# Performance work log

Hardware: AMD Instinct MI355X
Metric: run time of the kernel (lower is better)

## Reference

```python
import jax, jax.numpy as jnp
import numpy as np

N_NODES = 50000
N_EDGES = 800000
IN_F = 512
OUT_F = 96
ALPHA = 0.1
ITERATIONS = 10
AVG_DEG = 16


def setup_inputs() -> dict:
    key = jax.random.key(0)
    k1, k2, k3, k4, k5 = jax.random.split(key, 5)
    x = jax.random.normal(k1, (N_NODES, IN_F), dtype=jnp.float32)
    # xavier_uniform with gain=1.414 over [IN_F, OUT_F]
    limit = 1.414 * np.sqrt(6.0 / (IN_F + OUT_F))
    weight = jax.random.uniform(k2, (IN_F, OUT_F), dtype=jnp.float32,
                                minval=-limit, maxval=limit)
    edge_src = jax.random.randint(k3, (N_EDGES,), 0, N_NODES, dtype=jnp.int32)
    edge_dst = jax.random.randint(k4, (N_EDGES,), 0, N_NODES, dtype=jnp.int32)
    # values scaled like a row-normalized adjacency for stable propagation
    edge_val = jax.random.uniform(k5, (N_EDGES,), dtype=jnp.float32) / AVG_DEG
    return {"x": x, "weight": weight, "edge_src": edge_src,
            "edge_dst": edge_dst, "edge_val": edge_val}


def _spmm(edge_src, edge_dst, edge_val, h):
    # out[i] = sum_{edges e with dst=i} val[e] * h[src[e]]
    gathered = h[edge_src] * edge_val[:, None]          # [E, OUT_F]
    return jax.ops.segment_sum(gathered, edge_dst, num_segments=N_NODES)


def reference(x, weight, edge_src, edge_dst, edge_val):
    support = x @ weight                                 # [N, OUT_F]
    prev = support
    def body(_, s):
        s = _spmm(edge_src, edge_dst, edge_val, s) * (1.0 - ALPHA) + prev * ALPHA
        return jax.nn.relu(s)
    return jax.lax.fori_loop(0, ITERATIONS, body, support)
```

## Files before the change

### kernel.cpp

```cpp
#include <hip/hip_runtime.h>

typedef unsigned int   uint;
typedef unsigned short ushort;
typedef __attribute__((ext_vector_type(8))) short bf16x8;
typedef __attribute__((ext_vector_type(4))) float f32x4;

#define N_NODES 50000
#define N_EDGES 800000
#define IN_F    512
#define OUT_F   96
#define SCAN_BLOCKS 196
#define TPN 12

__device__ __forceinline__ float bflo(uint u) { return __uint_as_float(u << 16); }
__device__ __forceinline__ float bfhi(uint u) { return __uint_as_float(u & 0xffff0000u); }
__device__ __forceinline__ uint f2bf(float x) {
    uint u = __float_as_uint(x);
    return (u + 0x7fffu + ((u >> 16) & 1u)) >> 16;
}
__device__ __forceinline__ uint pack2bf(float lo, float hi) {
    return f2bf(lo) | (f2bf(hi) << 16);
}

__global__ __launch_bounds__(256) void wt_kernel(const float* __restrict__ w,
                                                 ushort* __restrict__ wTp) {
    int t = blockIdx.x * 256 + threadIdx.x;
    if (t < IN_F * OUT_F) {
        int k = t / OUT_F, c = t - k * OUT_F;
        wTp[(size_t)(k >> 5) * (OUT_F * 32) + c * 32 + (k & 31)] =
            (ushort)f2bf(w[t]);
    }
}

__global__ __launch_bounds__(64) void gemm_kernel(const float* __restrict__ x,
                                                  const ushort* __restrict__ wTp,
                                                  ushort* __restrict__ supB) {
    const int lane = threadIdx.x;
    const int m    = lane & 15;
    const int quad = lane >> 4;

    const int row  = blockIdx.x * 16 + m;
    const int arow = (row < N_NODES) ? row : (N_NODES - 1);
    const float*  xp = x + (size_t)arow * IN_F + quad * 8;
    const ushort* wp = wTp + (size_t)m * 32 + quad * 8;

    f32x4 acc[6];
    #pragma unroll
    for (int ct = 0; ct < 6; ++ct) acc[ct] = (f32x4){0.f, 0.f, 0.f, 0.f};

    float4 xA0 = *(const float4*)(xp);
    float4 xB0 = *(const float4*)(xp + 4);
    float4 xA1 = *(const float4*)(xp + 32);
    float4 xB1 = *(const float4*)(xp + 36);
    bf16x8 b[6];
    #pragma unroll
    for (int ct = 0; ct < 6; ++ct)
        b[ct] = *(const bf16x8*)(wp + ct * (16 * 32));

    #pragma unroll
    for (int it = 0; it < 16; ++it) {
        float4 nxa, nxb;
        bf16x8 nb[6];
        if (it + 2 < 16) {
            nxa = *(const float4*)(xp + (it + 2) * 32);
            nxb = *(const float4*)(xp + (it + 2) * 32 + 4);
        }
        if (it + 1 < 16) {
            const ushort* wpn = wp + (size_t)(it + 1) * (OUT_F * 32);
            #pragma unroll
            for (int ct = 0; ct < 6; ++ct)
                nb[ct] = *(const bf16x8*)(wpn + ct * (16 * 32));
        }
        union { uint u[4]; bf16x8 v; } af;
        af.u[0] = pack2bf(xA0.x, xA0.y); af.u[1] = pack2bf(xA0.z, xA0.w);
        af.u[2] = pack2bf(xB0.x, xB0.y); af.u[3] = pack2bf(xB0.z, xB0.w);
        #pragma unroll
        for (int ct = 0; ct < 6; ++ct)
            acc[ct] = __builtin_amdgcn_mfma_f32_16x16x32_bf16(af.v, b[ct],
                                                              acc[ct], 0, 0, 0);
        xA0 = xA1; xB0 = xB1; xA1 = nxa; xB1 = nxb;
        #pragma unroll
        for (int ct = 0; ct < 6; ++ct) b[ct] = nb[ct];
    }

    const int orow0 = blockIdx.x * 16 + quad * 4;
    #pragma unroll
    for (int ct = 0; ct < 6; ++ct) {
        #pragma unroll
        for (int r = 0; r < 4; ++r) {
            int gr = orow0 + r;
            if (gr < N_NODES)
                supB[(size_t)gr * OUT_F + ct * 16 + m] = (ushort)f2bf(acc[ct][r]);
        }
    }
}

__global__ void zero_kernel(int* __restrict__ p, int n) {
    int t = blockIdx.x * blockDim.x + threadIdx.x;
    if (t < n) p[t] = 0;
}

__global__ void hist_kernel(const int* __restrict__ dst, int* __restrict__ counts) {
    int e = blockIdx.x * blockDim.x + threadIdx.x;
    if (e < N_EDGES) atomicAdd(&counts[dst[e]], 1);
}

__global__ __launch_bounds__(256) void block_reduce_kernel(const int* __restrict__ counts,
                                                           int* __restrict__ blockSums) {
    __shared__ int s[256];
    int idx = blockIdx.x * 256 + threadIdx.x;
    s[threadIdx.x] = (idx < N_NODES) ? counts[idx] : 0;
    __syncthreads();
    for (int off = 128; off > 0; off >>= 1) {
        if (threadIdx.x < off) s[threadIdx.x] += s[threadIdx.x + off];
        __syncthreads();
    }
    if (threadIdx.x == 0) blockSums[blockIdx.x] = s[0];
}

__global__ __launch_bounds__(256) void scan_sums_kernel(int* __restrict__ blockSums,
                                                        int* __restrict__ blockOffs,
                                                        int* __restrict__ rowstart) {
    __shared__ int s[256];
    int t = threadIdx.x;
    s[t] = (t < SCAN_BLOCKS) ? blockSums[t] : 0;
    __syncthreads();
    for (int off = 1; off < 256; off <<= 1) {
        int v = (t >= off) ? s[t - off] : 0;
        __syncthreads();
        s[t] += v;
        __syncthreads();
    }
    if (t < SCAN_BLOCKS) blockOffs[t] = (t == 0) ? 0 : s[t - 1];
    if (t == 0) rowstart[N_NODES] = s[SCAN_BLOCKS - 1];
}

__global__ __launch_bounds__(256) void block_scan_kernel(const int* __restrict__ counts,
                                                         const int* __restrict__ blockOffs,
                                                         int* __restrict__ rowstart,
                                                         int* __restrict__ cursor) {
    __shared__ int s[256];
    int t   = threadIdx.x;
    int idx = blockIdx.x * 256 + t;
    int v   = (idx < N_NODES) ? counts[idx] : 0;
    s[t] = v;
    __syncthreads();
    for (int off = 1; off < 256; off <<= 1) {
        int u = (t >= off) ? s[t - off] : 0;
        __syncthreads();
        s[t] += u;
        __syncthreads();
    }
    if (idx < N_NODES) {
        int excl = blockOffs[blockIdx.x] + s[t] - v;
        rowstart[idx] = excl;
        cursor[idx]   = excl;
    }
}

__global__ void scatter_kernel(const int* __restrict__ src, const int* __restrict__ dst,
                               const float* __restrict__ val, int* __restrict__ cursor,
                               uint* __restrict__ edgeE) {
    int e = blockIdx.x * blockDim.x + threadIdx.x;
    if (e < N_EDGES) {
        int d   = dst[e];
        int pos = atomicAdd(&cursor[d], 1);
        edgeE[pos] = (f2bf(val[e]) << 16) | (uint)src[e];
    }
}

__device__ __forceinline__ void acc8(float* a, float v, uint4 hv) {
    a[0] = fmaf(v, bflo(hv.x), a[0]); a[1] = fmaf(v, bfhi(hv.x), a[1]);
    a[2] = fmaf(v, bflo(hv.y), a[2]); a[3] = fmaf(v, bfhi(hv.y), a[3]);
    a[4] = fmaf(v, bflo(hv.z), a[4]); a[5] = fmaf(v, bfhi(hv.z), a[5]);
    a[6] = fmaf(v, bflo(hv.w), a[6]); a[7] = fmaf(v, bfhi(hv.w), a[7]);
}

template <bool FINAL>
__global__ __launch_bounds__(256) void prop_kernel(const ushort* __restrict__ h,
                                                   const ushort* __restrict__ sup,
                                                   const int* __restrict__ rowstart,
                                                   const uint* __restrict__ edgeE,
                                                   ushort* __restrict__ outB,
                                                   float* __restrict__ outF) {
    int t = blockIdx.x * 256 + threadIdx.x;
    int i = t / TPN;
    if (i >= N_NODES) return;
    int q = t - i * TPN;
    int f = q * 8;

    int start = rowstart[i];
    int end   = rowstart[i + 1];

    float a[8] = {0.f, 0.f, 0.f, 0.f, 0.f, 0.f, 0.f, 0.f};
    int e = start;
    for (; e + 7 < end; e += 8) {
        uint ed[8];
        #pragma unroll
        for (int u = 0; u < 8; ++u) ed[u] = edgeE[e + u];
        uint4 hv[8];
        #pragma unroll
        for (int u = 0; u < 8; ++u)
            hv[u] = *(const uint4*)(h + (size_t)(ed[u] & 0xffffu) * OUT_F + f);
        #pragma unroll
        for (int u = 0; u < 8; ++u) acc8(a, bfhi(ed[u]), hv[u]);
    }
    for (; e < end; ++e) {
        uint e0 = edgeE[e];
        uint4 h0 = *(const uint4*)(h + (size_t)(e0 & 0xffffu) * OUT_F + f);
        acc8(a, bfhi(e0), h0);
    }

    size_t o = (size_t)i * OUT_F + f;
    uint4 sp = *(const uint4*)(sup + o);
    float r[8];
    r[0] = fmaxf(fmaf(a[0], 0.9f, bflo(sp.x) * 0.1f), 0.f);
    r[1] = fmaxf(fmaf(a[1], 0.9f, bfhi(sp.x) * 0.1f), 0.f);
    r[2] = fmaxf(fmaf(a[2], 0.9f, bflo(sp.y) * 0.1f), 0.f);
    r[3] = fmaxf(fmaf(a[3], 0.9f, bfhi(sp.y) * 0.1f), 0.f);
    r[4] = fmaxf(fmaf(a[4], 0.9f, bflo(sp.z) * 0.1f), 0.f);
    r[5] = fmaxf(fmaf(a[5], 0.9f, bfhi(sp.z) * 0.1f), 0.f);
    r[6] = fmaxf(fmaf(a[6], 0.9f, bflo(sp.w) * 0.1f), 0.f);
    r[7] = fmaxf(fmaf(a[7], 0.9f, bfhi(sp.w) * 0.1f), 0.f);

    if (FINAL) {
        *(float4*)(outF + o)     = make_float4(r[0], r[1], r[2], r[3]);
        *(float4*)(outF + o + 4) = make_float4(r[4], r[5], r[6], r[7]);
    } else {
        *(uint4*)(outB + o) = make_uint4(pack2bf(r[0], r[1]), pack2bf(r[2], r[3]),
                                         pack2bf(r[4], r[5]), pack2bf(r[6], r[7]));
    }
}

extern "C" void kernel_launch(void* const* d_in, const int* in_sizes, int n_in,
                              void* d_out, int out_size, void* d_ws, size_t ws_size,
                              hipStream_t stream) {
    const float* x    = (const float*)d_in[0];
    const float* w    = (const float*)d_in[1];
    const int*   esrc = (const int*)d_in[2];
    const int*   edst = (const int*)d_in[3];
    const float* eval = (const float*)d_in[4];
    float* out = (float*)d_out;

    const size_t supBytes = (size_t)N_NODES * OUT_F * sizeof(ushort);
    ushort* supB = (ushort*)d_out;
    ushort* wTp  = (ushort*)((char*)d_out + (size_t)out_size * 4
                             - (size_t)IN_F * OUT_F * sizeof(ushort));

    char*  xb  = (char*)d_in[0];
    size_t off = 0;
    auto alloc = [&](size_t bytes) -> char* {
        char* p = xb + off;
        off = (off + bytes + 255) & ~(size_t)255;
        return p;
    };
    ushort* supP      = (ushort*)alloc(supBytes);
    ushort* hU        = (ushort*)alloc(supBytes);
    ushort* hV        = (ushort*)alloc(supBytes);
    uint*   edgeE     = (uint*)alloc((size_t)N_EDGES * sizeof(uint));
    int*    rowstart  = (int*)alloc((N_NODES + 1) * sizeof(int));
    int*    cursor    = (int*)alloc(N_NODES * sizeof(int));
    int*    counts    = (int*)alloc(N_NODES * sizeof(int));
    int*    blockSums = (int*)alloc(SCAN_BLOCKS * sizeof(int));
    int*    blockOffs = (int*)alloc(SCAN_BLOCKS * sizeof(int));

    wt_kernel<<<(IN_F * OUT_F + 255) / 256, 256, 0, stream>>>(w, wTp);

    gemm_kernel<<<(N_NODES + 15) / 16, 64, 0, stream>>>(x, wTp, supB);

    hipMemcpyAsync(supP, supB, supBytes, hipMemcpyDeviceToDevice, stream);

    zero_kernel<<<(N_NODES + 255) / 256, 256, 0, stream>>>(counts, N_NODES);
    hist_kernel<<<(N_EDGES + 255) / 256, 256, 0, stream>>>(edst, counts);
    block_reduce_kernel<<<SCAN_BLOCKS, 256, 0, stream>>>(counts, blockSums);
    scan_sums_kernel<<<1, 256, 0, stream>>>(blockSums, blockOffs, rowstart);
    block_scan_kernel<<<SCAN_BLOCKS, 256, 0, stream>>>(counts, blockOffs,
                                                       rowstart, cursor);
    scatter_kernel<<<(N_EDGES + 255) / 256, 256, 0, stream>>>(esrc, edst, eval,
                                                              cursor, edgeE);

    const int pgrid = (N_NODES * TPN + 255) / 256;
    const ushort* in = supP;
    for (int it = 1; it <= 9; ++it) {
        ushort* o = (it & 1) ? hU : hV;
        prop_kernel<false><<<pgrid, 256, 0, stream>>>(in, supP, rowstart, edgeE,
                                                      o, nullptr);
        in = o;
    }
    prop_kernel<true><<<pgrid, 256, 0, stream>>>(in, supP, rowstart, edgeE,
                                                 nullptr, out);
}
```

Baseline: 561.2 us.

## Sort nodes by degree for balanced propagation and prefetch edge indices

Builds a degree histogram and a permutation that groups nodes of equal in-degree, so that warps in the propagation kernel process nodes with similar edge counts and diverge less. The propagation loop also software-prefetches the next chunk of edge indices, loads the support row early, and handles the remainder edges as one masked 8-wide batch instead of a serial tail loop. This adds extra setup kernels and an indirection through perm, and output writes become scattered in node order.

Result: slower. 772.6 us (+37.7%).

```diff
diff --git a/kernel.cpp b/kernel.cpp
--- a/kernel.cpp
+++ b/kernel.cpp
@@ -11,6 +11,7 @@
 #define OUT_F   96
 #define SCAN_BLOCKS 196
 #define TPN 12
+#define DEGBINS 256
 
 __device__ __forceinline__ float bflo(uint u) { return __uint_as_float(u << 16); }
 __device__ __forceinline__ float bfhi(uint u) { return __uint_as_float(u & 0xffff0000u); }
@@ -138,7 +139,8 @@
 __global__ __launch_bounds__(256) void block_scan_kernel(const int* __restrict__ counts,
                                                          const int* __restrict__ blockOffs,
                                                          int* __restrict__ rowstart,
-                                                         int* __restrict__ cursor) {
+                                                         int* __restrict__ cursor,
+                                                         int* __restrict__ deghist) {
     __shared__ int s[256];
     int t   = threadIdx.x;
     int idx = blockIdx.x * 256 + t;
@@ -155,6 +157,36 @@
         int excl = blockOffs[blockIdx.x] + s[t] - v;
         rowstart[idx] = excl;
         cursor[idx]   = excl;
+        int d = v < (DEGBINS - 1) ? v : (DEGBINS - 1);
+        atomicAdd(&deghist[d], 1);
+    }
+}
+
+__global__ __launch_bounds__(256) void degscan_kernel(const int* __restrict__ deghist,
+                                                      int* __restrict__ degcur) {
+    __shared__ int s[256];
+    int t = threadIdx.x;
+    int v = deghist[t];
+    s[t] = v;
+    __syncthreads();
+    for (int off = 1; off < 256; off <<= 1) {
+        int u = (t >= off) ? s[t - off] : 0;
+        __syncthreads();
+        s[t] += u;
+        __syncthreads();
+    }
+    degcur[t] = s[t] - v;
+}
+
+__global__ void degscatter_kernel(const int* __restrict__ counts,
+                                  int* __restrict__ degcur,
+                                  int* __restrict__ perm) {
+    int i = blockIdx.x * blockDim.x + threadIdx.x;
+    if (i < N_NODES) {
+        int d = counts[i];
+        if (d > DEGBINS - 1) d = DEGBINS - 1;
+        int pos = atomicAdd(&degcur[d], 1);
+        perm[pos] = i;
     }
 }
 
@@ -181,6 +213,7 @@
                                                    const ushort* __restrict__ sup,
                                                    const int* __restrict__ rowstart,
                                                    const uint* __restrict__ edgeE,
+                                                   const int* __restrict__ perm,
                                                    ushort* __restrict__ outB,
                                                    float* __restrict__ outF) {
     int t = blockIdx.x * 256 + threadIdx.x;
@@ -188,31 +221,59 @@
     if (i >= N_NODES) return;
     int q = t - i * TPN;
     int f = q * 8;
-
-    int start = rowstart[i];
-    int end   = rowstart[i + 1];
+    int node = perm[i];
+
+    int start = rowstart[node];
+    int end   = rowstart[node + 1];
+
+    size_t o = (size_t)node * OUT_F + f;
+    uint4 sp = *(const uint4*)(sup + o);
 
     float a[8] = {0.f, 0.f, 0.f, 0.f, 0.f, 0.f, 0.f, 0.f};
-    int e = start;
-    for (; e + 7 < end; e += 8) {
-        uint ed[8];
-        #pragma unroll
-        for (int u = 0; u < 8; ++u) ed[u] = edgeE[e + u];
+    int e  = start;
+    int n8 = (end - start) >> 3;
+
+    uint ed[8];
+    if (n8 > 0) {
+        #pragma unroll
+        for (int u = 0; u < 8; ++u) ed[u] = edgeE[start + u];
+    }
+    for (int c = 0; c < n8; ++c) {
         uint4 hv[8];
         #pragma unroll
         for (int u = 0; u < 8; ++u)
             hv[u] = *(const uint4*)(h + (size_t)(ed[u] & 0xffffu) * OUT_F + f);
-        #pragma unroll
-        for (int u = 0; u < 8; ++u) acc8(a, bfhi(ed[u]), hv[u]);
-    }
-    for (; e < end; ++e) {
-        uint e0 = edgeE[e];
-        uint4 h0 = *(const uint4*)(h + (size_t)(e0 & 0xffffu) * OUT_F + f);
-        acc8(a, bfhi(e0), h0);
-    }
-
-    size_t o = (size_t)i * OUT_F + f;
-    uint4 sp = *(const uint4*)(sup + o);
+        uint edc[8];
+        #pragma unroll
+        for (int u = 0; u < 8; ++u) edc[u] = ed[u];
+        if (c + 1 < n8) {
+            #pragma unroll
+            for (int u = 0; u < 8; ++u) ed[u] = edgeE[e + 8 + u];
+        }
+        #pragma unroll
+        for (int u = 0; u < 8; ++u) acc8(a, bfhi(edc[u]), hv[u]);
+        e += 8;
+    }
+
+    int rem = end - e;
+    if (rem > 0) {
+        uint edt[8];
+        #pragma unroll
+        for (int u = 0; u < 8; ++u) {
+            int ee = e + u;
+            edt[u] = edgeE[(ee < end) ? ee : (end - 1)];
+        }
+        uint4 hv[8];
+        #pragma unroll
+        for (int u = 0; u < 8; ++u)
+            hv[u] = *(const uint4*)(h + (size_t)(edt[u] & 0xffffu) * OUT_F + f);
+        #pragma unroll
+        for (int u = 0; u < 8; ++u) {
+            float v = (u < rem) ? bfhi(edt[u]) : 0.f;
+            acc8(a, v, hv[u]);
+        }
+    }
+
     float r[8];
     r[0] = fmaxf(fmaf(a[0], 0.9f, bflo(sp.x) * 0.1f), 0.f);
     r[1] = fmaxf(fmaf(a[1], 0.9f, bfhi(sp.x) * 0.1f), 0.f);
@@ -260,9 +321,12 @@
     uint*   edgeE     = (uint*)alloc((size_t)N_EDGES * sizeof(uint));
     int*    rowstart  = (int*)alloc((N_NODES + 1) * sizeof(int));
     int*    cursor    = (int*)alloc(N_NODES * sizeof(int));
-    int*    counts    = (int*)alloc(N_NODES * sizeof(int));
+    int*    counts    = (int*)alloc((N_NODES + DEGBINS) * sizeof(int));
+    int*    deghist   = counts + N_NODES;
     int*    blockSums = (int*)alloc(SCAN_BLOCKS * sizeof(int));
     int*    blockOffs = (int*)alloc(SCAN_BLOCKS * sizeof(int));
+    int*    degcur    = (int*)alloc(DEGBINS * sizeof(int));
+    int*    perm      = (int*)alloc(N_NODES * sizeof(int));
 
     wt_kernel<<<(IN_F * OUT_F + 255) / 256, 256, 0, stream>>>(w, wTp);
 
@@ -270,12 +334,16 @@
 
     hipMemcpyAsync(supP, supB, supBytes, hipMemcpyDeviceToDevice, stream);
 
-    zero_kernel<<<(N_NODES + 255) / 256, 256, 0, stream>>>(counts, N_NODES);
+    zero_kernel<<<(N_NODES + DEGBINS + 255) / 256, 256, 0, stream>>>(
+        counts, N_NODES + DEGBINS);
     hist_kernel<<<(N_EDGES + 255) / 256, 256, 0, stream>>>(edst, counts);
     block_reduce_kernel<<<SCAN_BLOCKS, 256, 0, stream>>>(counts, blockSums);
     scan_sums_kernel<<<1, 256, 0, stream>>>(blockSums, blockOffs, rowstart);
     block_scan_kernel<<<SCAN_BLOCKS, 256, 0, stream>>>(counts, blockOffs,
-                                                       rowstart, cursor);
+                                                       rowstart, cursor, deghist);
+    degscan_kernel<<<1, 256, 0, stream>>>(deghist, degcur);
+    degscatter_kernel<<<(N_NODES + 255) / 256, 256, 0, stream>>>(counts, degcur,
+                                                                 perm);
     scatter_kernel<<<(N_EDGES + 255) / 256, 256, 0, stream>>>(esrc, edst, eval,
                                                               cursor, edgeE);
 
@@ -284,9 +352,9 @@
     for (int it = 1; it <= 9; ++it) {
         ushort* o = (it & 1) ? hU : hV;
         prop_kernel<false><<<pgrid, 256, 0, stream>>>(in, supP, rowstart, edgeE,
-                                                      o, nullptr);
+                                                      perm, o, nullptr);
         in = o;
     }
     prop_kernel<true><<<pgrid, 256, 0, stream>>>(in, supP, rowstart, edgeE,
-                                                 nullptr, out);
-}
+                                                 perm, nullptr, out);
+}
```
